# Kernel optimization log

Hardware: AMD Instinct MI355X
Metric: run time of the kernel (lower is better)

## Reference

```python
import jax, jax.numpy as jnp
import numpy as np


def _filters(bmt):
    # bmt: (L,) low-pass h(-m1..m2). dec_lo = flip(h); g_tilde = flip(h)*(-1)^j;
    # dec_hi = flip(g_tilde)  (matches bmt_h / bmt_g_tilde / bmt_g in the torch code)
    L = bmt.shape[0]
    signs = 1.0 - 2.0 * (jnp.arange(L) % 2).astype(bmt.dtype)  # (+1,-1,+1,...)
    dec_lo = jnp.flip(bmt)
    g_tilde = dec_lo * signs
    dec_hi = jnp.flip(g_tilde)
    return dec_lo, dec_hi


def _conv_stride2(xp, w):
    # xp: (B,1,Npad), w: (L,) -> cross-correlation, stride 2, valid (== torch conv1d)
    return jax.lax.conv_general_dilated(xp, w[None, None, :], window_strides=(2,), padding='VALID')


def _dwt(x, dec_lo, dec_hi, m1, m2):
    # x: (B,K,N) -> (a, d) each (B,K,N//2). Periodic padding:
    # pad_periodic(x,n1,n2)[i] = x[(i-n1) mod N]  ==  jnp.pad mode='wrap'.
    B, K, N = x.shape
    xr = x.reshape(B * K, 1, N)
    xa = jnp.pad(xr, ((0, 0), (0, 0), (m1, m2)), mode='wrap')
    a = _conv_stride2(xa, dec_lo)
    xd = jnp.pad(xr, ((0, 0), (0, 0), (m2 - 1, m1 + 1)), mode='wrap')
    d = _conv_stride2(xd, dec_hi)
    return a.reshape(B, K, N // 2), d.reshape(B, K, N // 2)


def setup_inputs() -> dict:
    key = jax.random.key(0)
    k1, k2 = jax.random.split(key)
    x = jax.random.normal(k1, (32, 1024, 1024), dtype=jnp.float32)
    bmt = jax.random.normal(k2, (8,), dtype=jnp.float32)
    return {"x": x, "bmt": bmt, "m1": 3, "m2": 4}


def reference(x, bmt, m1, m2):
    # 2D fast wavelet transform in square format (Wav_2d_sqformat)
    dec_lo, dec_hi = _filters(bmt)
    cA, cD = _dwt(x, dec_lo, dec_hi, m1, m2)                       # rows filtered
    cAA, cAD = _dwt(cA.swapaxes(1, 2), dec_lo, dec_hi, m1, m2)     # cols of cA
    cDA, cDD = _dwt(cD.swapaxes(1, 2), dec_lo, dec_hi, m1, m2)     # cols of cD
    cAA, cAD = cAA.swapaxes(1, 2), cAD.swapaxes(1, 2)
    cDA, cDD = cDA.swapaxes(1, 2), cDD.swapaxes(1, 2)
    top = jnp.concatenate([cAA, cAD], axis=2)
    bot = jnp.concatenate([cDA, cDD], axis=2)
    return jnp.concatenate([top, bot], axis=1)  # (B,N,N)
```

## Files before the change

kernel.cpp:

```cpp
#include <hip/hip_runtime.h>

#define NN 1024
#define HH 512
#define TR 32
#define TC 32
#define S1R 70
#define XC 72
#define XST 73
#define NF4 18
#define NLD ((S1R * NF4 + 255) / 256)

__global__ __launch_bounds__(256, 4) void dwt2d_fused(const float* __restrict__ x,
                                                      const float* __restrict__ bmt,
                                                      float* __restrict__ out) {
    __shared__ float  Xs[S1R][XST];
    __shared__ float2 AD[S1R][TC + 2];

    const int tid = threadIdx.x;
    const int b  = blockIdx.z;
    const int R0 = blockIdx.y * TR;
    const int C0 = blockIdx.x * TC;

    float lo[8], hi[8];
#pragma unroll
    for (int j = 0; j < 8; ++j) lo[j] = bmt[7 - j];
#pragma unroll
    for (int j = 0; j < 8; ++j) { float v = bmt[j]; hi[j] = (j & 1) ? v : -v; }

    const float* xb = x + (size_t)b * NN * NN;
    const int rbase = 2 * R0 - 3;
    const int pb    = 2 * C0 - 4;

    float4 v[NLD];
    int    su[NLD], stc[NLD];
#pragma unroll
    for (int k = 0; k < NLD; ++k) {
        int idx = tid + 256 * k;
        unsigned uu = (unsigned)idx / 18u;
        int tt = idx - 18 * (int)uu;
        su[k] = (int)uu; stc[k] = tt;
        int row = (rbase + (int)uu) & (NN - 1);
        int gc  = (pb + 4 * tt) & (NN - 1);
        v[k] = *(const float4*)(xb + ((size_t)row << 10) + gc);
    }
#pragma unroll
    for (int k = 0; k < NLD; ++k) {
        int idx = tid + 256 * k;
        if (idx < S1R * NF4) {
            int u = su[k], t4 = 4 * stc[k];
            Xs[u][t4 + 0] = v[k].x;
            Xs[u][t4 + 1] = v[k].y;
            Xs[u][t4 + 2] = v[k].z;
            Xs[u][t4 + 3] = v[k].w;
        }
    }
    __syncthreads();

    for (int pos = tid; pos < S1R * 8; pos += 256) {
        int u  = pos >> 3;
        int c0 = (pos & 7) * 4;
        float p[14];
#pragma unroll
        for (int t = 0; t < 14; ++t) p[t] = Xs[u][2 * c0 + 1 + t];
#pragma unroll
        for (int m = 0; m < 4; ++m) {
            float a = 0.f, d = 0.f;
#pragma unroll
            for (int j = 0; j < 8; ++j) {
                float w = p[2 * m + j];
                a += lo[j] * w;
                d += hi[j] * w;
            }
            AD[u][c0 + m] = make_float2(a, d);
        }
    }
    __syncthreads();

    const int cg = tid & 7;
    const int r  = tid >> 3;
    float aa[4] = {0,0,0,0}, ad[4] = {0,0,0,0}, da[4] = {0,0,0,0}, dd[4] = {0,0,0,0};
#pragma unroll
    for (int j = 0; j < 8; ++j) {
        float2 q[4];
#pragma unroll
        for (int i = 0; i < 4; ++i) q[i] = AD[2 * r + j][4 * cg + i];
        float l = lo[j], h = hi[j];
#pragma unroll
        for (int i = 0; i < 4; ++i) {
            aa[i] += l * q[i].x;
            ad[i] += h * q[i].x;
            da[i] += l * q[i].y;
            dd[i] += h * q[i].y;
        }
    }
    float* ob = out + (size_t)b * NN * NN;
    const int orow = R0 + r;
    const int ocol = C0 + 4 * cg;
    *(float4*)(ob + (size_t)orow * NN + ocol)             = make_float4(aa[0], aa[1], aa[2], aa[3]);
    *(float4*)(ob + (size_t)orow * NN + ocol + HH)        = make_float4(ad[0], ad[1], ad[2], ad[3]);
    *(float4*)(ob + (size_t)(orow + HH) * NN + ocol)      = make_float4(da[0], da[1], da[2], da[3]);
    *(float4*)(ob + (size_t)(orow + HH) * NN + ocol + HH) = make_float4(dd[0], dd[1], dd[2], dd[3]);
}

extern "C" void kernel_launch(void* const* d_in, const int* in_sizes, int n_in,
                              void* d_out, int out_size, void* d_ws, size_t ws_size,
                              hipStream_t stream) {
    const float* x   = (const float*)d_in[0];
    const float* bmt = (const float*)d_in[1];
    float* out = (float*)d_out;
    const int B = in_sizes[0] / (NN * NN);
    dim3 grid(HH / TC, HH / TR, B);
    dwt2d_fused<<<grid, 256, 0, stream>>>(x, bmt, out);
}
```

Measured before the change: 233.0 us.

## Use packed FP32 FMAs and split A/D shared arrays for vectorized LDS access

Replaces scalar FMAs in both filtering stages with inline-asm v_pk_fma_f32, computing the low and high outputs together with op_sel broadcasts. The shared tile is shifted by one column so that 8-byte vector reads line up. The interleaved float2 AD buffer becomes separate A and D arrays, so the column pass can use 16-byte LDS loads. The aim is to halve VALU instruction count and cut LDS instruction count in what looks like a memory-bound kernel, at the cost of inline asm and a trickier shared-memory layout.

```diff
diff --git a/kernel.cpp b/kernel.cpp
--- a/kernel.cpp
+++ b/kernel.cpp
@@ -5,40 +5,56 @@
 #define TR 32
 #define TC 32
 #define S1R 70
-#define XC 72
-#define XST 73
+#define XST 74
 #define NF4 18
 #define NLD ((S1R * NF4 + 255) / 256)
+#define ADS 36
+
+typedef float f2  __attribute__((ext_vector_type(2)));
+typedef float f4v __attribute__((ext_vector_type(4)));
+
+__device__ __forceinline__ void pk_fma_blo(f2& acc, f2 ab, f2 w) {
+    asm("v_pk_fma_f32 %0, %1, %2, %0 op_sel:[0,0,0] op_sel_hi:[1,0,1]"
+        : "+v"(acc) : "v"(ab), "v"(w));
+}
+__device__ __forceinline__ void pk_fma_bhi(f2& acc, f2 ab, f2 w) {
+    asm("v_pk_fma_f32 %0, %1, %2, %0 op_sel:[0,1,0] op_sel_hi:[1,1,1]"
+        : "+v"(acc) : "v"(ab), "v"(w));
+}
 
 __global__ __launch_bounds__(256, 4) void dwt2d_fused(const float* __restrict__ x,
                                                       const float* __restrict__ bmt,
                                                       float* __restrict__ out) {
-    __shared__ float  Xs[S1R][XST];
-    __shared__ float2 AD[S1R][TC + 2];
+    __shared__ float Xs[S1R][XST];
+    __shared__ float As[S1R][ADS];
+    __shared__ float Ds[S1R][ADS];
 
     const int tid = threadIdx.x;
     const int b  = blockIdx.z;
     const int R0 = blockIdx.y * TR;
     const int C0 = blockIdx.x * TC;
 
-    float lo[8], hi[8];
+    f2 lohi[8];
 #pragma unroll
-    for (int j = 0; j < 8; ++j) lo[j] = bmt[7 - j];
-#pragma unroll
-    for (int j = 0; j < 8; ++j) { float v = bmt[j]; hi[j] = (j & 1) ? v : -v; }
+    for (int j = 0; j < 8; ++j) {
+        float l = bmt[7 - j];
+        float v = bmt[j];
+        f2 p; p.x = l; p.y = (j & 1) ? v : -v;
+        lohi[j] = p;
+    }
 
     const float* xb = x + (size_t)b * NN * NN;
     const int rbase = 2 * R0 - 3;
     const int pb    = 2 * C0 - 4;
 
     float4 v[NLD];
-    int    su[NLD], stc[NLD];
+    int    su[NLD], st4[NLD];
 #pragma unroll
     for (int k = 0; k < NLD; ++k) {
         int idx = tid + 256 * k;
         unsigned uu = (unsigned)idx / 18u;
         int tt = idx - 18 * (int)uu;
-        su[k] = (int)uu; stc[k] = tt;
+        su[k] = (int)uu; st4[k] = tt;
         int row = (rbase + (int)uu) & (NN - 1);
         int gc  = (pb + 4 * tt) & (NN - 1);
         v[k] = *(const float4*)(xb + ((size_t)row << 10) + gc);
@@ -47,11 +63,12 @@
     for (int k = 0; k < NLD; ++k) {
         int idx = tid + 256 * k;
         if (idx < S1R * NF4) {
-            int u = su[k], t4 = 4 * stc[k];
-            Xs[u][t4 + 0] = v[k].x;
-            Xs[u][t4 + 1] = v[k].y;
-            Xs[u][t4 + 2] = v[k].z;
-            Xs[u][t4 + 3] = v[k].w;
+            int u = su[k];
+            int q = 4 * st4[k] - 1;
+            if (q >= 0) Xs[u][q] = v[k].x;
+            f2 yz; yz.x = v[k].y; yz.y = v[k].z;
+            *(f2*)&Xs[u][q + 1] = yz;
+            Xs[u][q + 3] = v[k].w;
         }
     }
     __syncthreads();
@@ -59,47 +76,59 @@
     for (int pos = tid; pos < S1R * 8; pos += 256) {
         int u  = pos >> 3;
         int c0 = (pos & 7) * 4;
-        float p[14];
+        const f2* wrow = (const f2*)&Xs[u][2 * c0];
+        f2 w2[7];
 #pragma unroll
-        for (int t = 0; t < 14; ++t) p[t] = Xs[u][2 * c0 + 1 + t];
+        for (int t = 0; t < 7; ++t) w2[t] = wrow[t];
+        f2 accs[4];
 #pragma unroll
         for (int m = 0; m < 4; ++m) {
-            float a = 0.f, d = 0.f;
+            f2 acc; acc.x = 0.f; acc.y = 0.f;
 #pragma unroll
-            for (int j = 0; j < 8; ++j) {
-                float w = p[2 * m + j];
-                a += lo[j] * w;
-                d += hi[j] * w;
+            for (int s = 0; s < 4; ++s) {
+                pk_fma_blo(acc, lohi[2 * s],     w2[m + s]);
+                pk_fma_bhi(acc, lohi[2 * s + 1], w2[m + s]);
             }
-            AD[u][c0 + m] = make_float2(a, d);
+            accs[m] = acc;
         }
+        f4v va, vd;
+        va.x = accs[0].x; va.y = accs[1].x; va.z = accs[2].x; va.w = accs[3].x;
+        vd.x = accs[0].y; vd.y = accs[1].y; vd.z = accs[2].y; vd.w = accs[3].y;
+        *(f4v*)&As[u][c0] = va;
+        *(f4v*)&Ds[u][c0] = vd;
     }
     __syncthreads();
 
     const int cg = tid & 7;
     const int r  = tid >> 3;
-    float aa[4] = {0,0,0,0}, ad[4] = {0,0,0,0}, da[4] = {0,0,0,0}, dd[4] = {0,0,0,0};
+    f2 acc0[4], acc1[4];
+#pragma unroll
+    for (int i = 0; i < 4; ++i) {
+        acc0[i].x = 0.f; acc0[i].y = 0.f;
+        acc1[i].x = 0.f; acc1[i].y = 0.f;
+    }
 #pragma unroll
     for (int j = 0; j < 8; ++j) {
-        float2 q[4];
-#pragma unroll
-        for (int i = 0; i < 4; ++i) q[i] = AD[2 * r + j][4 * cg + i];
-        float l = lo[j], h = hi[j];
-#pragma unroll
-        for (int i = 0; i < 4; ++i) {
-            aa[i] += l * q[i].x;
-            ad[i] += h * q[i].x;
-            da[i] += l * q[i].y;
-            dd[i] += h * q[i].y;
-        }
+        f4v qa = *(const f4v*)&As[2 * r + j][4 * cg];
+        f4v qd = *(const f4v*)&Ds[2 * r + j][4 * cg];
+        f2 lh = lohi[j];
+        f2 a01 = qa.xy, a23 = qa.zw, d01 = qd.xy, d23 = qd.zw;
+        pk_fma_blo(acc0[0], lh, a01);
+        pk_fma_bhi(acc0[1], lh, a01);
+        pk_fma_blo(acc0[2], lh, a23);
+        pk_fma_bhi(acc0[3], lh, a23);
+        pk_fma_blo(acc1[0], lh, d01);
+        pk_fma_bhi(acc1[1], lh, d01);
+        pk_fma_blo(acc1[2], lh, d23);
+        pk_fma_bhi(acc1[3], lh, d23);
     }
     float* ob = out + (size_t)b * NN * NN;
     const int orow = R0 + r;
     const int ocol = C0 + 4 * cg;
-    *(float4*)(ob + (size_t)orow * NN + ocol)             = make_float4(aa[0], aa[1], aa[2], aa[3]);
-    *(float4*)(ob + (size_t)orow * NN + ocol + HH)        = make_float4(ad[0], ad[1], ad[2], ad[3]);
-    *(float4*)(ob + (size_t)(orow + HH) * NN + ocol)      = make_float4(da[0], da[1], da[2], da[3]);
-    *(float4*)(ob + (size_t)(orow + HH) * NN + ocol + HH) = make_float4(dd[0], dd[1], dd[2], dd[3]);
+    *(float4*)(ob + (size_t)orow * NN + ocol)             = make_float4(acc0[0].x, acc0[1].x, acc0[2].x, acc0[3].x);
+    *(float4*)(ob + (size_t)orow * NN + ocol + HH)        = make_float4(acc0[0].y, acc0[1].y, acc0[2].y, acc0[3].y);
+    *(float4*)(ob + (size_t)(orow + HH) * NN + ocol)      = make_float4(acc1[0].x, acc1[1].x, acc1[2].x, acc1[3].x);
+    *(float4*)(ob + (size_t)(orow + HH) * NN + ocol + HH) = make_float4(acc1[0].y, acc1[1].y, acc1[2].y, acc1[3].y);
 }
 
 extern "C" void kernel_launch(void* const* d_in, const int* in_sizes, int n_in,
```

Result: no change. 231.2 us (-0.8%).
